# Optimization experiments

Measured on AMD Instinct MI355X. Metric: run time of the kernel, lower is better.

Reference implementation:

```python
import jax, jax.numpy as jnp
import numpy as np
from jax import lax

ALPHA, OMEGA, EPSILON, THETA, W_MASK = 2.1, 14.0, 1.0, 0.5, 10.0


def setup_inputs() -> dict:
    key = jax.random.key(0)
    k1, k2 = jax.random.split(key)
    shape = (64, 68, 128, 128)
    pred = jax.random.uniform(k1, shape, dtype=jnp.float32)
    landmark = jax.random.uniform(k2, shape, dtype=jnp.float32)
    return {"pred": pred, "landmark": landmark}


def _weight_mask(landmark):
    # replicate cv2: round(heatmap*255), 3x3 rect dilation (max filter), threshold at 0.2*h
    hm = jnp.round(landmark * 255.0)
    dil = lax.reduce_window(hm, -jnp.inf, lax.max,
                            window_dimensions=(1, 1, 3, 3),
                            window_strides=(1, 1, 1, 1),
                            padding='SAME')
    h = landmark.shape[2]  # h == w in the original thresholding
    return (dil >= h * 0.2).astype(landmark.dtype)


def _awing(pred, landmark):
    diff = jnp.abs(pred - landmark)
    asl = ALPHA - landmark                      # alpha - y, elementwise exponent
    tde = THETA / EPSILON
    T1 = tde ** asl
    T2 = tde ** (asl - 1.0)
    A = OMEGA / (1.0 + T1) * asl * T2 / EPSILON
    C = THETA * A - OMEGA * jnp.log1p(T1)
    return jnp.where(diff < THETA,
                     OMEGA * jnp.log1p((diff / EPSILON) ** asl),
                     A * diff - C)


def reference(pred, landmark):
    M = _weight_mask(landmark)
    loss = _awing(pred, landmark) * (W_MASK * M + 1.0)
    return jnp.mean(loss)
```

## Files before the change

kernel.cpp:

```cpp
#include <hip/hip_runtime.h>

constexpr int H = 128, W = 128;
constexpr int IMG = H * W;
constexpr int STRIP = 32;
constexpr int STRIPS = H / STRIP;

__device__ __forceinline__ float max3f(float a, float b, float c) {
    return fmaxf(fmaxf(a, b), c);
}
__device__ __forceinline__ float exp2_hw(float x) { return __builtin_amdgcn_exp2f(x); }
__device__ __forceinline__ float log2_hw(float x) { return __builtin_amdgcn_logf(x); }
__device__ __forceinline__ float ln1p_fast(float x) {
    return log2_hw(1.0f + x) * 0.69314718055994530942f;
}

__global__ __launch_bounds__(256, 4) void awing_partial(
    const float* __restrict__ pred,
    const float* __restrict__ lmk,
    float* __restrict__ part)
{
    __shared__ __align__(16) float s[(STRIP + 2) * W];
    __shared__ float wsum[4];

    const int tid  = threadIdx.x;
    const int img  = blockIdx.x >> 2;
    const int st   = blockIdx.x & 3;
    const int row0 = st * STRIP;
    const float* li = lmk  + (size_t)img * IMG;
    const float* pi = pred + (size_t)img * IMG;

    for (int s4 = tid; s4 < (STRIP + 2) * W / 4; s4 += 256) {
        int lr = s4 >> 5;
        int c4 = s4 & 31;
        int gr = row0 - 1 + lr;
        float4 v = make_float4(-1e30f, -1e30f, -1e30f, -1e30f);
        if (gr >= 0 && gr < H) v = ((const float4*)li)[gr * 32 + c4];
        ((float4*)s)[s4] = v;
    }
    __syncthreads();

    float acc = 0.0f;
#pragma unroll
    for (int it = 0; it < 4; ++it) {
        int e  = it * 1024 + tid * 4;
        int rl = e >> 7;
        int c  = e & 127;

        float4 p4 = ((const float4*)pi)[(row0 + rl) * 32 + (c >> 2)];

        int b0 = rl * W + c;
        float4 a4 = *(const float4*)&s[b0];
        float4 b4 = *(const float4*)&s[b0 + W];
        float4 d4 = *(const float4*)&s[b0 + 2 * W];

        float aL, bL, cL, aR, bR, cR;
        if (c > 0)     { aL = s[b0 - 1];     bL = s[b0 + W - 1];     cL = s[b0 + 2*W - 1]; }
        else           { aL = bL = cL = -1e30f; }
        if (c < W - 4) { aR = s[b0 + 4];     bR = s[b0 + W + 4];     cR = s[b0 + 2*W + 4]; }
        else           { aR = bR = cR = -1e30f; }

        float vL = max3f(aL, bL, cL);
        float v0 = max3f(a4.x, b4.x, d4.x);
        float v1 = max3f(a4.y, b4.y, d4.y);
        float v2 = max3f(a4.z, b4.z, d4.z);
        float v3 = max3f(a4.w, b4.w, d4.w);
        float vR = max3f(aR, bR, cR);
        float mm[4] = { max3f(vL, v0, v1), max3f(v0, v1, v2),
                        max3f(v1, v2, v3), max3f(v2, v3, vR) };
        float yy[4] = { b4.x, b4.y, b4.z, b4.w };
        float pp[4] = { p4.x, p4.y, p4.z, p4.w };

#pragma unroll
        for (int j = 0; j < 4; ++j) {
            float y    = yy[j];
            float diff = fabsf(pp[j] - y);
            float asl  = 2.1f - y;
            float T1   = exp2_hw(-asl);
            float invd = 1.0f / (1.0f + T1);
            float A    = 14.0f * asl * (2.0f * T1) * invd;
            float C    = 0.5f * A - 14.0f * ln1p_fast(T1);
            float pw   = exp2_hw(asl * log2_hw(diff));
            float lo   = 14.0f * ln1p_fast(pw);
            float hi   = A * diff - C;
            float lossv = (diff < 0.5f) ? lo : hi;
            float wgt  = (rintf(mm[j] * 255.0f) >= 25.6f) ? 11.0f : 1.0f;
            acc = fmaf(lossv, wgt, acc);
        }
    }

#pragma unroll
    for (int off = 32; off > 0; off >>= 1) acc += __shfl_down(acc, off, 64);
    if ((tid & 63) == 0) wsum[tid >> 6] = acc;
    __syncthreads();
    if (tid == 0) part[blockIdx.x] = (wsum[0] + wsum[1]) + (wsum[2] + wsum[3]);
}

__global__ void final_reduce(const float* __restrict__ part, int n,
                             float* __restrict__ out, double inv_total)
{
    __shared__ double sd[4];
    int tid = threadIdx.x;
    double a = 0.0;
    for (int i = tid; i < n; i += 256) a += (double)part[i];
#pragma unroll
    for (int off = 32; off > 0; off >>= 1) a += __shfl_down(a, off, 64);
    if ((tid & 63) == 0) sd[tid >> 6] = a;
    __syncthreads();
    if (tid == 0) out[0] = (float)((sd[0] + sd[1] + sd[2] + sd[3]) * inv_total);
}

extern "C" void kernel_launch(void* const* d_in, const int* in_sizes, int n_in,
                              void* d_out, int out_size, void* d_ws, size_t ws_size,
                              hipStream_t stream)
{
    const float* pred = (const float*)d_in[0];
    const float* lmk  = (const float*)d_in[1];
    float* part = (float*)d_ws;
    int total   = in_sizes[0];
    int nimg    = total / IMG;
    int nblocks = nimg * STRIPS;

    awing_partial<<<nblocks, 256, 0, stream>>>(pred, lmk, part);
    final_reduce<<<1, 256, 0, stream>>>(part, nblocks, (float*)d_out,
                                        1.0 / (double)total);
}
```

Before: 546.3 us.

## Share transcendentals across loss branches and exchange dilation halos via lane shuffles

The loss is rewritten so both branches use one log2, one exp2, one log2(1+E) and one hardware reciprocal: the exponent is chosen per branch, and the constant C is folded into the fused multiply-add. This cuts the per-element transcendental count, which appears to dominate the kernel's cost. The left and right halo values for the 3x3 max are now taken from neighbouring lanes with shuffles instead of extra LDS loads. Out-of-image rows are clamped to edge replication rather than filled with a sentinel, which gives the same result under a max. Two smaller changes: the rounding threshold is replaced by an equivalent direct comparison, and the launch-bounds occupancy hint is raised from 4 to 8.

```diff
diff --git a/kernel.cpp b/kernel.cpp
--- a/kernel.cpp
+++ b/kernel.cpp
@@ -10,11 +10,9 @@
 }
 __device__ __forceinline__ float exp2_hw(float x) { return __builtin_amdgcn_exp2f(x); }
 __device__ __forceinline__ float log2_hw(float x) { return __builtin_amdgcn_logf(x); }
-__device__ __forceinline__ float ln1p_fast(float x) {
-    return log2_hw(1.0f + x) * 0.69314718055994530942f;
-}
+__device__ __forceinline__ float rcp_hw(float x)  { return __builtin_amdgcn_rcpf(x); }
 
-__global__ __launch_bounds__(256, 4) void awing_partial(
+__global__ __launch_bounds__(256, 8) void awing_partial(
     const float* __restrict__ pred,
     const float* __restrict__ lmk,
     float* __restrict__ part)
@@ -29,15 +27,17 @@
     const float* li = lmk  + (size_t)img * IMG;
     const float* pi = pred + (size_t)img * IMG;
 
-    for (int s4 = tid; s4 < (STRIP + 2) * W / 4; s4 += 256) {
+    for (int s4 = tid; s4 < (STRIP + 2) * (W / 4); s4 += 256) {
         int lr = s4 >> 5;
         int c4 = s4 & 31;
         int gr = row0 - 1 + lr;
-        float4 v = make_float4(-1e30f, -1e30f, -1e30f, -1e30f);
-        if (gr >= 0 && gr < H) v = ((const float4*)li)[gr * 32 + c4];
-        ((float4*)s)[s4] = v;
+        gr = min(max(gr, 0), H - 1);
+        ((float4*)s)[s4] = ((const float4*)li)[gr * (W / 4) + c4];
     }
     __syncthreads();
+
+    const bool leftEdge  = (tid & 31) == 0;
+    const bool rightEdge = (tid & 31) == 31;
 
     float acc = 0.0f;
 #pragma unroll
@@ -53,18 +53,15 @@
         float4 b4 = *(const float4*)&s[b0 + W];
         float4 d4 = *(const float4*)&s[b0 + 2 * W];
 
-        float aL, bL, cL, aR, bR, cR;
-        if (c > 0)     { aL = s[b0 - 1];     bL = s[b0 + W - 1];     cL = s[b0 + 2*W - 1]; }
-        else           { aL = bL = cL = -1e30f; }
-        if (c < W - 4) { aR = s[b0 + 4];     bR = s[b0 + W + 4];     cR = s[b0 + 2*W + 4]; }
-        else           { aR = bR = cR = -1e30f; }
-
-        float vL = max3f(aL, bL, cL);
         float v0 = max3f(a4.x, b4.x, d4.x);
         float v1 = max3f(a4.y, b4.y, d4.y);
         float v2 = max3f(a4.z, b4.z, d4.z);
         float v3 = max3f(a4.w, b4.w, d4.w);
-        float vR = max3f(aR, bR, cR);
+        float vL = __shfl_up(v3, 1, 64);
+        float vR = __shfl_down(v0, 1, 64);
+        vL = leftEdge  ? v0 : vL;
+        vR = rightEdge ? v3 : vR;
+
         float mm[4] = { max3f(vL, v0, v1), max3f(v0, v1, v2),
                         max3f(v1, v2, v3), max3f(v2, v3, vR) };
         float yy[4] = { b4.x, b4.y, b4.z, b4.w };
@@ -73,17 +70,18 @@
 #pragma unroll
         for (int j = 0; j < 4; ++j) {
             float y    = yy[j];
-            float diff = fabsf(pp[j] - y);
+            float d    = fabsf(pp[j] - y);
             float asl  = 2.1f - y;
-            float T1   = exp2_hw(-asl);
-            float invd = 1.0f / (1.0f + T1);
-            float A    = 14.0f * asl * (2.0f * T1) * invd;
-            float C    = 0.5f * A - 14.0f * ln1p_fast(T1);
-            float pw   = exp2_hw(asl * log2_hw(diff));
-            float lo   = 14.0f * ln1p_fast(pw);
-            float hi   = A * diff - C;
-            float lossv = (diff < 0.5f) ? lo : hi;
-            float wgt  = (rintf(mm[j] * 255.0f) >= 25.6f) ? 11.0f : 1.0f;
+            bool  lo   = d < 0.5f;
+            float L    = log2_hw(d);
+            float beta = lo ? asl * L : -asl;
+            float E    = exp2_hw(beta);
+            float S    = 1.0f + E;
+            float G    = log2_hw(S);
+            float A    = 28.0f * asl * E * rcp_hw(S);
+            float Asel = lo ? 0.0f : A;
+            float lossv = fmaf(Asel, d - 0.5f, 9.704060527839234f * G);
+            float wgt  = (mm[j] * 255.0f >= 25.5f) ? 11.0f : 1.0f;
             acc = fmaf(lossv, wgt, acc);
         }
     }
```

New measurement: 542.4 us. About the same (-0.7%).
